# Optimization experiments

Measured on AMD Instinct MI355X. Metric: run time of the kernel, lower is better.

## Reference

```python
import jax, jax.numpy as jnp
import numpy as np
from jax import lax

B = 8192
HS = 64        # hidden_size (output channels)
HS4 = HS + 4   # internal channel count (68)
K = 3          # conv kernel size


def setup_inputs() -> dict:
    key = jax.random.key(0)
    ks = jax.random.split(key, 16)
    def n(k, shape, s=1.0):
        return jax.random.normal(k, shape, dtype=jnp.float32) * s
    return {
        "x": n(ks[0], (B, HS, 6, 6)),
        "cell": n(ks[1], (B, 2)),
        "interspace_coord": n(ks[2], (B, 2, 6, 6)),
        "conv1_w": n(ks[3], (HS4, HS4, K, K), 0.05),
        "conv1_b": n(ks[4], (HS4,), 0.05),
        "conv3_w": n(ks[5], (HS4, HS4, K, K), 0.05),
        "conv3_b": n(ks[6], (HS4,), 0.05),
        "lin5_w": n(ks[7], (9 * HS, HS4 * 25), 0.02),
        "lin5_b": n(ks[8], (9 * HS,), 0.02),
        "lin4_w": n(ks[9], (9 * HS, HS4 * 16), 0.02),
        "lin4_b": n(ks[10], (9 * HS,), 0.02),
        "lin3_w": n(ks[11], (9 * HS, HS4 * 9), 0.02),
        "lin3_b": n(ks[12], (9 * HS,), 0.02),
        "final_w": n(ks[13], (HS, 9 * HS), 0.02),
        "final_b": n(ks[14], (HS,), 0.02),
    }


def _conv(z, w, b):
    # torch Conv2d with padding=k//2, stride 1 == SAME conv, NCHW/OIHW
    y = lax.conv_general_dilated(z, w, (1, 1), 'SAME',
                                 dimension_numbers=('NCHW', 'OIHW', 'NCHW'))
    return y + b[None, :, None, None]


def _corners(z, ws):
    # four corner windows, stacked on a new leading axis (corner-major)
    H, W = z.shape[-2:]
    return jnp.stack([z[..., :ws, :ws],
                      z[..., :ws, W - ws:],
                      z[..., H - ws:, :ws],
                      z[..., H - ws:, W - ws:]], axis=0)


def reference(x, cell, interspace_coord,
              conv1_w, conv1_b, conv3_w, conv3_b,
              lin5_w, lin5_b, lin4_w, lin4_b, lin3_w, lin3_b,
              final_w, final_b):
    Bn = x.shape[0]
    new_cell = jnp.broadcast_to(cell.reshape(Bn, -1)[:, :, None, None],
                                (Bn, 2, 6, 6))
    lins = {5: (lin5_w, lin5_b), 4: (lin4_w, lin4_b), 3: (lin3_w, lin3_b)}
    for ws in (5, 4, 3):
        z = jnp.concatenate([x, new_cell, interspace_coord], axis=1)  # [B,68,6,6]
        z = _corners(z, ws).reshape(-1, HS4, ws, ws)                  # [4B,68,ws,ws]
        z = jnp.sin(z) + jnp.cos(z)
        z = jax.nn.relu(_conv(z, conv1_w, conv1_b))
        z = jnp.sin(z) + jnp.cos(z)
        z = jax.nn.relu(_conv(z, conv3_w, conv3_b)).reshape(4, Bn, -1)
        Wl, bl = lins[ws]
        z = jax.nn.relu(z @ Wl.T + bl).reshape(4, Bn, HS, 3, 3)
        m = jnp.concatenate([z[0], z[1]], axis=-1)   # [B,64,3,6]
        n = jnp.concatenate([z[2], z[3]], axis=-1)
        x = jnp.concatenate([m, n], axis=-2)          # [B,64,6,6]
    ew = 3
    c = _corners(x, ew)                               # [4,B,64,3,3]
    c = c.reshape(4 * Bn, -1) @ final_w.T + final_b   # [4B,64]
    c = c.reshape(Bn, HS, 2, 2)                       # same flat-order reshape as torch
    xc = x[:, :, ew - 1:ew + 1, ew - 1:ew + 1]        # center 2x2
    return (xc * c).reshape(Bn, HS, -1)
```

## Files before the change

### kernel.cpp

```cpp
#include <hip/hip_runtime.h>
#include <hip/hip_bf16.h>
#include <cstdint>
#include <cstddef>

#define BN 8192
#define MTOT 32768

using bf16 = __hip_bfloat16;
typedef float f32x4 __attribute__((ext_vector_type(4)));
typedef short short8 __attribute__((ext_vector_type(8)));

__device__ __forceinline__ bf16 f2b(float v) { return __float2bfloat16(v); }
__device__ __forceinline__ float b2f(bf16 v) { return __bfloat162float(v); }
__device__ __forceinline__ float sincos_sum(float x) {
    return 1.41421356237f * __sinf(x + 0.78539816340f);
}


__global__ __launch_bounds__(256)
void zprep_block(const float* __restrict__ xF, const float* __restrict__ cell,
                 const float* __restrict__ isc, bf16* __restrict__ Z,
                 int m0g, int CM)
{
    constexpr int KD = 1728, KTRUE = 1700;
    const int b = blockIdx.x, tid = threadIdx.x;
    __shared__ float s[68][37];

    for (int i = tid; i < 64 * 36; i += 256) {
        int ic = i / 36, off = i % 36;
        s[ic][off] = sincos_sum(xF[((size_t)b * 64 + ic) * 36 + off]);
    }
    if (tid < 2) {
        float t = sincos_sum(cell[b * 2 + tid]);
        #pragma unroll
        for (int off = 0; off < 36; off++) s[64 + tid][off] = t;
    }
    if (tid >= 64 && tid < 136) {
        int j = tid - 64;
        int ic = j / 36, off = j % 36;
        s[66 + ic][off] = sincos_sum(isc[((size_t)b * 2 + ic) * 36 + off]);
    }
    __syncthreads();

    for (int i = tid; i < 4 * (KD / 8); i += 256) {
        int q = i / (KD / 8), j8 = i % (KD / 8);
        int gm = q * BN + b;
        if (gm < m0g || gm >= m0g + CM) continue;
        int kbase = j8 * 8;
        short8 pack;
        #pragma unroll
        for (int u = 0; u < 8; u++) {
            int k = kbase + u;
            float v = 0.f;
            if (k < KTRUE) {
                int pi = k / 68, ic = k % 68;
                int r = (q >> 1) + pi / 5;
                int c = (q & 1) + pi % 5;
                v = s[ic][r * 6 + c];
            }
            bf16 bv = f2b(v);
            pack[u] = *reinterpret_cast<short*>(&bv);
        }
        *reinterpret_cast<short8*>(&Z[(size_t)(gm - m0g) * KD + kbase]) = pack;
    }
}

template<int WSv>
__device__ __forceinline__ bf16 conv_elem(const float* __restrict__ src, int n, int k)
{
    constexpr int KTRUE = 68 * WSv * WSv;
    float v = 0.f;
    if (n < KTRUE && k < KTRUE) {
        int po = n / 68, oc = n % 68, ro = po / WSv, co = po % WSv;
        int pi = k / 68, ic = k % 68, ri = pi / WSv, ci = pi % WSv;
        int kr = ri - ro + 1, kc = ci - co + 1;
        if (kr >= 0 && kr < 3 && kc >= 0 && kc < 3)
            v = src[((oc * 68 + ic) * 3 + kr) * 3 + kc];
    }
    return f2b(v);
}
template<int WSv>
__device__ __forceinline__ bf16 lin_elem(const float* __restrict__ wl, int n, int k)
{
    constexpr int KTRUE = 68 * WSv * WSv;
    float v = 0.f;
    if (n < 576 && k < KTRUE) {
        int pi = k / 68, ic = k % 68;
        v = wl[(size_t)n * KTRUE + ic * (WSv * WSv) + pi];
    }
    return f2b(v);
}

__global__ void megabuild(const float* __restrict__ c1w, const float* __restrict__ c3w,
                          const float* __restrict__ l5w, const float* __restrict__ l4w,
                          const float* __restrict__ l3w, const float* __restrict__ fw,
                          const float* __restrict__ c1b, const float* __restrict__ c3b,
                          const float* __restrict__ bl5, const float* __restrict__ bl4,
                          const float* __restrict__ bl3, const float* __restrict__ bfin,
                          const float* __restrict__ cell, const float* __restrict__ isc,
                          bf16* __restrict__ w1d5, bf16* __restrict__ w3d5,
                          bf16* __restrict__ w1d4, bf16* __restrict__ w3d4,
                          bf16* __restrict__ w1d3, bf16* __restrict__ w3d3,
                          bf16* __restrict__ wl5p, bf16* __restrict__ wl4p,
                          bf16* __restrict__ wl3p, bf16* __restrict__ wfp,
                          float* __restrict__ bias,
                          bf16* __restrict__ Z4, bf16* __restrict__ Z3)
{
    constexpr unsigned S0 = 2u*1792*1728, S1 = 2u*1152*1088, S2 = 2u*640*640;
    constexpr unsigned S3 = 640u*1728, S4 = 640u*1088, S5 = 640u*640;
    constexpr unsigned S6 = 128u*576, S7 = 9216;
    constexpr unsigned S8 = 4u*8192*16*4, S9 = 4u*8192*9*4, S10 = 32768u*28;
    constexpr unsigned O1=S0, O2=O1+S1, O3=O2+S2, O4=O3+S3, O5=O4+S4, O6=O5+S5,
                       O7=O6+S6, O8=O7+S7, O9=O8+S8, O10=O9+S9, OT=O10+S10;
    unsigned e = blockIdx.x * 256u + threadIdx.x;
    if (e >= OT) return;
    if (e < O1) {
        constexpr unsigned per = 1792u*1728;
        unsigned i = (e < per) ? e : e - per;
        bf16* dst = (e < per) ? w1d5 : w3d5;
        const float* src = (e < per) ? c1w : c3w;
        dst[i] = conv_elem<5>(src, (int)(i / 1728u), (int)(i % 1728u));
    } else if (e < O2) {
        unsigned i0 = e - O1; constexpr unsigned per = 1152u*1088;
        unsigned i = (i0 < per) ? i0 : i0 - per;
        bf16* dst = (i0 < per) ? w1d4 : w3d4;
        const float* src = (i0 < per) ? c1w : c3w;
        dst[i] = conv_elem<4>(src, (int)(i / 1088u), (int)(i % 1088u));
    } else if (e < O3) {
        unsigned i0 = e - O2; constexpr unsigned per = 640u*640;
        unsigned i = (i0 < per) ? i0 : i0 - per;
        bf16* dst = (i0 < per) ? w1d3 : w3d3;
        const float* src = (i0 < per) ? c1w : c3w;
        dst[i] = conv_elem<3>(src, (int)(i / 640u), (int)(i % 640u));
    } else if (e < O4) {
        unsigned i = e - O3;
        wl5p[i] = lin_elem<5>(l5w, (int)(i / 1728u), (int)(i % 1728u));
    } else if (e < O5) {
        unsigned i = e - O4;
        wl4p[i] = lin_elem<4>(l4w, (int)(i / 1088u), (int)(i % 1088u));
    } else if (e < O6) {
        unsigned i = e - O5;
        wl3p[i] = lin_elem<3>(l3w, (int)(i / 640u), (int)(i % 640u));
    } else if (e < O7) {
        unsigned i = e - O6, n = i / 576u, k = i % 576u;
        wfp[i] = (n < 64u) ? f2b(fw[n * 576u + k]) : f2b(0.f);
    } else if (e < O8) {
        int i = (int)(e - O7);
        float v = 0.f;
        if (i < 1792)      { int n = i;        if (n < 1700) v = c1b[n % 68]; }
        else if (i < 3584) { int n = i - 1792; if (n < 1700) v = c3b[n % 68]; }
        else if (i < 4736) { int n = i - 3584; if (n < 1088) v = c1b[n % 68]; }
        else if (i < 5888) { int n = i - 4736; if (n < 1088) v = c3b[n % 68]; }
        else if (i < 6528) { int n = i - 5888; if (n < 612)  v = c1b[n % 68]; }
        else if (i < 7168) { int n = i - 6528; if (n < 612)  v = c3b[n % 68]; }
        else if (i < 7808) { int n = i - 7168; if (n < 576)  v = bl5[n]; }
        else if (i < 8448) { int n = i - 7808; if (n < 576)  v = bl4[n]; }
        else if (i < 9088) { int n = i - 8448; if (n < 576)  v = bl3[n]; }
        else               { int n = i - 9088; if (n < 64)   v = bfin[n]; }
        bias[i] = v;
    } else if (e < O9) {
        unsigned i = e - O8;
        int j = (int)(i & 3u); i >>= 2;
        int pi = (int)(i & 15u); i >>= 4;
        int b = (int)(i & 8191u); int q = (int)(i >> 13);
        float t;
        if (j < 2) t = cell[b * 2 + j];
        else {
            int r = (q >> 1) * 2 + pi / 4, c = (q & 1) * 2 + pi % 4;
            t = isc[((size_t)b * 2 + (j - 2)) * 36 + r * 6 + c];
        }
        Z4[((size_t)q * BN + b) * 1088 + pi * 68 + 64 + j] = f2b(sincos_sum(t));
    } else if (e < O10) {
        unsigned i = e - O9;
        int j = (int)(i & 3u); i >>= 2;
        int pi = (int)(i % 9u); i /= 9u;
        int b = (int)(i & 8191u); int q = (int)(i >> 13);
        float t;
        if (j < 2) t = cell[b * 2 + j];
        else {
            int r = (q >> 1) * 3 + pi / 3, c = (q & 1) * 3 + pi % 3;
            t = isc[((size_t)b * 2 + (j - 2)) * 36 + r * 6 + c];
        }
        Z3[((size_t)q * BN + b) * 640 + pi * 68 + 64 + j] = f2b(sincos_sum(t));
    } else {
        unsigned i = e - O10;
        int m = (int)(i / 28u), t = (int)(i % 28u);
        Z3[(size_t)m * 640 + 612 + t] = f2b(0.f);
    }
}

__device__ __forceinline__ void gload_lds16(const bf16* g, const bf16* lds_wave_base)
{
    unsigned off = (unsigned)(uintptr_t)lds_wave_base;
    off = __builtin_amdgcn_readfirstlane(off);
    __builtin_amdgcn_global_load_lds((const __attribute__((address_space(1))) unsigned int*)g,
                                     (__attribute__((address_space(3))) unsigned int*)off,
                                     16, 0, 0);
}

__device__ __forceinline__ int imin(int a, int b) { return a < b ? a : b; }
__device__ __forceinline__ int imax(int a, int b) { return a > b ? a : b; }

template<int EPI, int WS, int WN, int WIDE>
__global__ __launch_bounds__(512, 4)
void gemm8(const bf16* __restrict__ A, const bf16* __restrict__ Bm, int KD,
           const float* __restrict__ bias, int ntiles, int mtiles,
           bf16* __restrict__ C, int ldc, int nlimit,
           int m0g, bf16* __restrict__ znext)
{
    constexpr int BMc = WIDE ? 128 : 256;
    constexpr int BNc = WIDE ? 256 : 128;
    constexpr int NWN = WIDE ? 4 : 2;
    __shared__ bf16 As[3][BMc * 32];
    __shared__ bf16 Bs[3][BNc * 32];
    const int tid = threadIdx.x;
    const int wave = tid >> 6, lane = tid & 63;
    const int l15 = lane & 15, lq = lane >> 4;
    const int wr = (wave / NWN) * 64, wc = (wave % NWN) * 64;

    const int xcd = blockIdx.x & 7, local = blockIdx.x >> 3;
    const int mloc = mtiles >> 3;
    const int PP = (mloc >= 4) ? 4 : mloc;
    const int grp = ntiles * PP;
    const int p = local / grp, rem = local % grp;
    const int n_idx = rem / PP, mi = rem % PP;
    const int m_idx = xcd * mloc + p * PP + mi;
    const int n0 = n_idx * BNc, m0 = m_idx * BMc;

    int s0b = 0, s0e = KD, s1b = 0, s1e = 0, s2b = 0, s2e = 0;
    if (WS > 0) {
        int po_lo = imin(n0 / 68, WS * WS - 1);
        int po_hi = imin((n0 + BNc - 1) / 68, WS * WS - 1);
        int ro_lo = po_lo / WS, ro_hi = po_hi / WS;
        int r_lo = imax(ro_lo - 1, 0), r_hi = imin(ro_hi + 1, WS - 1);
        int ci_lo = 0, ci_hi = WS - 1;
        if (ro_lo == ro_hi) {
            ci_lo = imax(po_lo % WS - 1, 0);
            ci_hi = imin(po_hi % WS + 1, WS - 1);
        }
        if (ci_lo == 0 && ci_hi == WS - 1) {
            s0b = (r_lo * WS * 68) & ~31;
            s0e = imin(KD, ((r_hi + 1) * WS * 68 + 31) & ~31);
        } else {
            s0b = ((r_lo * WS + ci_lo) * 68) & ~31;
            s0e = imin(KD, (((r_lo * WS + ci_hi + 1) * 68) + 31) & ~31);
            if (r_hi > r_lo) {
                s1b = (((r_lo + 1) * WS + ci_lo) * 68) & ~31;
                s1e = imin(KD, ((((r_lo + 1) * WS + ci_hi + 1) * 68) + 31) & ~31);
            }
            if (r_hi > r_lo + 1) {
                s2b = (((r_lo + 2) * WS + ci_lo) * 68) & ~31;
                s2e = imin(KD, ((((r_lo + 2) * WS + ci_hi + 1) * 68) + 31) & ~31);
            }
        }
    }
    const int c0 = (s0e - s0b) >> 5;
    const int c1 = c0 + ((s1e - s1b) >> 5);
    const int nt = c1 + ((s2e - s2b) >> 5);
    auto k0_of = [&](int t2) -> int {
        int k = s0b + (t2 << 5);
        if (t2 >= c0) k = s1b + ((t2 - c0) << 5);
        if (t2 >= c1) k = s2b + ((t2 - c1) << 5);
        return k;
    };

    const int srow = tid >> 2;
    const int scx = (tid & 3) ^ ((srow >> 1) & 3);
    const int sOff = srow * 32 + (tid & 3) * 8;
    const int swz = (lq ^ ((l15 >> 1) & 3)) * 8;
    const int offA0 = (wr + l15) * 32 + swz;
    const int offB0 = (wc + l15) * 32 + swz;

    const bf16* aSrc = A + (size_t)(m0 + srow) * KD + scx * 8;
    const bf16* bSrc = Bm + (size_t)(n0 + srow) * KD + scx * 8;

    auto stageAll = [&](int k0, int buf) {
        if (WIDE) {
            gload_lds16(aSrc + k0, &As[buf][sOff]);
            gload_lds16(bSrc + k0, &Bs[buf][sOff]);
            gload_lds16(bSrc + k0 + (size_t)128 * KD, &Bs[buf][sOff + 4096]);
        } else {
            gload_lds16(aSrc + k0, &As[buf][sOff]);
            gload_lds16(aSrc + k0 + (size_t)128 * KD, &As[buf][sOff + 4096]);
            gload_lds16(bSrc + k0, &Bs[buf][sOff]);
        }
    };

    f32x4 acc[4][4];
    #pragma unroll
    for (int i = 0; i < 4; i++)
        #pragma unroll
        for (int j = 0; j < 4; j++) { f32x4 z = {0.f, 0.f, 0.f, 0.f}; acc[i][j] = z; }

    {
        stageAll(k0_of(0), 0);
        if (nt > 1) stageAll(k0_of(1), 1);
        __syncthreads();
    }

    for (int t = 0; t < nt; ++t) {
        const int cur = t % 3;
        const int nx = (t + 2) % 3;
        const bool pf = (t + 2) < nt;

        const bf16* Ac = &As[cur][0];
        const bf16* Bc = &Bs[cur][0];

        short8 af[4], bg[4];
        #pragma unroll
        for (int i = 0; i < 4; i++) af[i] = *(const short8*)&Ac[offA0 + i * 512];
        #pragma unroll
        for (int j = 0; j < 4; j++) bg[j] = *(const short8*)&Bc[offB0 + j * 512];

        if (pf) stageAll(k0_of(t + 2), nx);

        __builtin_amdgcn_s_setprio(1);
        #pragma unroll
        for (int i = 0; i < 4; i++)
            #pragma unroll
            for (int j = 0; j < 4; j++)
                acc[i][j] = __builtin_amdgcn_mfma_f32_16x16x32_bf16(af[i], bg[j], acc[i][j], 0, 0, 0);
        __builtin_amdgcn_s_setprio(0);

        if (pf) asm volatile("s_waitcnt vmcnt(3)" ::: "memory");
        else    asm volatile("s_waitcnt vmcnt(0)" ::: "memory");
        __builtin_amdgcn_s_barrier();
    }

    float bj[4];
    #pragma unroll
    for (int j = 0; j < 4; j++) bj[j] = bias[n0 + wc + j * 16 + l15];

    #pragma unroll
    for (int i = 0; i < 4; i++) {
        #pragma unroll
        for (int j = 0; j < 4; j++) {
            int n = n0 + wc + j * 16 + l15;
            #pragma unroll
            for (int r = 0; r < 4; r++) {
                int m = m0 + wr + i * 16 + lq * 4 + r;
                float v = acc[i][j][r];
                if (EPI == 0) {
                    if (n < nlimit) {
                        v += bj[j]; v = fmaxf(v, 0.f); v = sincos_sum(v);
                        C[(size_t)m * ldc + n] = f2b(v);
                    }
                } else if (EPI == 1) {
                    if (n < nlimit) {
                        v += bj[j]; v = fmaxf(v, 0.f);
                        C[(size_t)m * ldc + n] = f2b(v);
                    }
                } else {
                    if (n < 576) {
                        v += bj[j]; v = fmaxf(v, 0.f);
                        bf16 tv = f2b(sincos_sum(v));
                        int gm = m0g + m;
                        int q = gm >> 13, b = gm & (BN - 1);
                        int ch = n / 9, p2 = n % 9;
                        int R = p2 / 3 + (q >> 1) * 3, Cc = p2 % 3 + (q & 1) * 3;
                        constexpr int OFF = 6 - WN;
                        constexpr int KDN = (WN == 4) ? 1088 : 640;
                        #pragma unroll
                        for (int qr = 0; qr < 2; qr++) {
                            int rr = R - OFF * qr;
                            if (rr < 0 || rr >= WN) continue;
                            #pragma unroll
                            for (int qc = 0; qc < 2; qc++) {
                                int cc = Cc - OFF * qc;
                                if (cc < 0 || cc >= WN) continue;
                                int pi = rr * WN + cc;
                                znext[((size_t)((qr * 2 + qc) * BN + b)) * KDN + pi * 68 + ch] = tv;
                            }
                        }
                    }
                }
            }
        }
    }
}

template<int EPI, int WS, int WN>
__global__ __launch_bounds__(256)
void gemm_bt(const bf16* __restrict__ A, const bf16* __restrict__ Bm, int KD,
             const float* __restrict__ bias, int ntiles,
             bf16* __restrict__ C, int ldc, int nlimit,
             int m0g, bf16* __restrict__ znext,
             const bf16* __restrict__ afin_xc, float* __restrict__ outp)
{
    __shared__ bf16 As[128 * 32];
    __shared__ bf16 Bs[128 * 32];
    const int tid = threadIdx.x;
    const int wave = tid >> 6, lane = tid & 63;
    const int l15 = lane & 15, lq = lane >> 4;
    const int wr = (wave >> 1) * 64, wc = (wave & 1) * 64;

    const int id = blockIdx.x;
    const int mt8 = (int)gridDim.x / (ntiles * 8);
    const int xcd = id & 7, local = id >> 3;
    const int m_idx = xcd * mt8 + local / ntiles;
    const int n_idx = local % ntiles;
    const int n0 = n_idx * 128, m0 = m_idx * 128;

    int nspans = 1, sbeg[4], send[4];
    sbeg[0] = 0; send[0] = KD;
    if (WS > 0) {
        int po_lo = imin(n0 / 68, WS * WS - 1);
        int po_hi = imin((n0 + 127) / 68, WS * WS - 1);
        int ro_lo = po_lo / WS, ro_hi = po_hi / WS;
        int r_lo = imax(ro_lo - 1, 0), r_hi = imin(ro_hi + 1, WS - 1);
        int ci_lo = 0, ci_hi = WS - 1;
        if (ro_lo == ro_hi) {
            ci_lo = imax(po_lo % WS - 1, 0);
            ci_hi = imin(po_hi % WS + 1, WS - 1);
        }
        if (ci_lo == 0 && ci_hi == WS - 1) {
            sbeg[0] = (r_lo * WS * 68) & ~31;
            send[0] = imin(KD, ((r_hi + 1) * WS * 68 + 31) & ~31);
        } else {
            nspans = 0;
            for (int ri = r_lo; ri <= r_hi; ri++) {
                sbeg[nspans] = ((ri * WS + ci_lo) * 68) & ~31;
                send[nspans] = imin(KD, (((ri * WS + ci_hi + 1) * 68) + 31) & ~31);
                nspans++;
            }
        }
    }

    float bj[4];
    #pragma unroll
    for (int j = 0; j < 4; j++) bj[j] = bias[n0 + wc + j * 16 + l15];

    const bf16* Ab = A + (size_t)m0 * KD;
    const bf16* Bb = Bm + (size_t)n0 * KD;
    const int srow = tid >> 2, scol = (tid & 3) * 8;
    const bf16* aG0 = Ab + (size_t)srow * KD + scol;
    const bf16* aG1 = Ab + (size_t)(srow + 64) * KD + scol;
    const bf16* bG0 = Bb + (size_t)srow * KD + scol;
    const bf16* bG1 = Bb + (size_t)(srow + 64) * KD + scol;
    const bf16* lA0 = &As[wave * 512];
    const bf16* lA1 = &As[2048 + wave * 512];
    const bf16* lB0 = &Bs[wave * 512];
    const bf16* lB1 = &Bs[2048 + wave * 512];

    f32x4 acc[4][4];
    #pragma unroll
    for (int i = 0; i < 4; i++)
        #pragma unroll
        for (int j = 0; j < 4; j++) { f32x4 z = {0.f, 0.f, 0.f, 0.f}; acc[i][j] = z; }

    for (int s = 0; s < nspans; s++) {
        for (int k0 = sbeg[s]; k0 < send[s]; k0 += 32) {
            gload_lds16(aG0 + k0, lA0);
            gload_lds16(aG1 + k0, lA1);
            gload_lds16(bG0 + k0, lB0);
            gload_lds16(bG1 + k0, lB1);
            __syncthreads();
            short8 af[4], bg[4];
            #pragma unroll
            for (int i = 0; i < 4; i++) af[i] = *(const short8*)&As[(wr + i * 16 + l15) * 32 + lq * 8];
            #pragma unroll
            for (int j = 0; j < 4; j++) bg[j] = *(const short8*)&Bs[(wc + j * 16 + l15) * 32 + lq * 8];
            #pragma unroll
            for (int i = 0; i < 4; i++)
                #pragma unroll
                for (int j = 0; j < 4; j++)
                    acc[i][j] = __builtin_amdgcn_mfma_f32_16x16x32_bf16(af[i], bg[j], acc[i][j], 0, 0, 0);
            __syncthreads();
        }
    }

    #pragma unroll
    for (int i = 0; i < 4; i++) {
        #pragma unroll
        for (int j = 0; j < 4; j++) {
            int n = n0 + wc + j * 16 + l15;
            #pragma unroll
            for (int r = 0; r < 4; r++) {
                int m = m0 + wr + i * 16 + lq * 4 + r;
                float v = acc[i][j][r];
                if (EPI == 0) {
                    if (n < nlimit) {
                        v += bj[j]; v = fmaxf(v, 0.f); v = sincos_sum(v);
                        C[(size_t)m * ldc + n] = f2b(v);
                    }
                } else if (EPI == 1) {
                    if (n < nlimit) {
                        v += bj[j]; v = fmaxf(v, 0.f);
                        C[(size_t)m * ldc + n] = f2b(v);
                    }
                } else if (EPI == 2) {
                    if (n < 576) {
                        v += bj[j]; v = fmaxf(v, 0.f);
                        bf16 t = f2b(sincos_sum(v));
                        int gm = m0g + m;
                        int q = gm >> 13, b = gm & (BN - 1);
                        int ch = n / 9, p = n % 9;
                        int R = p / 3 + (q >> 1) * 3, Cc = p % 3 + (q & 1) * 3;
                        constexpr int OFF = 6 - WN;
                        constexpr int KDN = (WN == 4) ? 1088 : 640;
                        #pragma unroll
                        for (int qr = 0; qr < 2; qr++) {
                            int rr = R - OFF * qr;
                            if (rr < 0 || rr >= WN) continue;
                            #pragma unroll
                            for (int qc = 0; qc < 2; qc++) {
                                int cc = Cc - OFF * qc;
                                if (cc < 0 || cc >= WN) continue;
                                int pi = rr * WN + cc;
                                znext[((size_t)((qr * 2 + qc) * BN + b)) * KDN + pi * 68 + ch] = t;
                            }
                        }
                    }
                } else {
                    if (n < 64) {
                        v += bj[j];
                        int gm = m0g + m;
                        int f = gm * 64 + n;
                        int b2 = f >> 8, rem = f & 255;
                        int ch2 = rem >> 2, ii = (rem >> 1) & 1, jj = rem & 1;
                        int qq = ii * 2 + jj;
                        const int offt[4] = {8, 6, 2, 0};
                        float xc = b2f(afin_xc[((size_t)qq * BN + b2) * 576 + ch2 * 9 + offt[qq]]);
                        outp[f] = v * xc;
                    }
                }
            }
        }
    }
}

extern "C" void kernel_launch(void* const* d_in, const int* in_sizes, int n_in,
                              void* d_out, int out_size, void* d_ws, size_t ws_size,
                              hipStream_t stream)
{
    const float* x    = (const float*)d_in[0];
    const float* cell = (const float*)d_in[1];
    const float* isc  = (const float*)d_in[2];
    const float* c1w  = (const float*)d_in[3];
    const float* c1b  = (const float*)d_in[4];
    const float* c3w  = (const float*)d_in[5];
    const float* c3b  = (const float*)d_in[6];
    const float* l5w  = (const float*)d_in[7];
    const float* l5b  = (const float*)d_in[8];
    const float* l4w  = (const float*)d_in[9];
    const float* l4b  = (const float*)d_in[10];
    const float* l3w  = (const float*)d_in[11];
    const float* l3b  = (const float*)d_in[12];
    const float* fw   = (const float*)d_in[13];
    const float* fb   = (const float*)d_in[14];

    char* base = (char*)d_ws;
    size_t cur = 0;
    auto take = [&](size_t bytes) -> char* {
        char* r = base + cur; cur += (bytes + 255) & ~(size_t)255; return r;
    };

    const size_t Z4B = (size_t)MTOT * 1088 * 2;
    const size_t Z3B = (size_t)MTOT * 640 * 2;
    const size_t AFB = (size_t)MTOT * 576 * 2;
    size_t wbytes = 2 * (1792ull * 1728 + 1152ull * 1088 + 640ull * 640) * 2
                  + (640ull * 1728 + 640ull * 1088 + 640ull * 640) * 2
                  + 128ull * 576 * 2 + 9216ull * 4 + 64 * 256;
    auto need = [&](int nc) -> size_t {
        return Z4B + Z3B + AFB + wbytes + 2 * ((size_t)(MTOT / nc) * 1728 * 2);
    };
    int nchunk = (ws_size >= need(1)) ? 1 : (ws_size >= need(2)) ? 2
               : (ws_size >= need(4)) ? 4 : (ws_size >= need(8)) ? 8 : 16;

    bf16* Z4   = (bf16*)take(Z4B);
    bf16* Z3   = (bf16*)take(Z3B);
    bf16* afinb = (bf16*)take(AFB);
    bf16* w1d5 = (bf16*)take(1792ull * 1728 * 2);
    bf16* w3d5 = (bf16*)take(1792ull * 1728 * 2);
    bf16* w1d4 = (bf16*)take(1152ull * 1088 * 2);
    bf16* w3d4 = (bf16*)take(1152ull * 1088 * 2);
    bf16* w1d3 = (bf16*)take(640ull * 640 * 2);
    bf16* w3d3 = (bf16*)take(640ull * 640 * 2);
    bf16* wl5p = (bf16*)take(640ull * 1728 * 2);
    bf16* wl4p = (bf16*)take(640ull * 1088 * 2);
    bf16* wl3p = (bf16*)take(640ull * 640 * 2);
    bf16* wfp  = (bf16*)take(128ull * 576 * 2);
    float* biasb = (float*)take(9216ull * 4);
    int CM = MTOT / nchunk;
    int mt = CM / 128;
    int mt2 = CM / 256;
    bf16* Za = (bf16*)take((size_t)CM * 1728 * 2);
    bf16* Zb = (bf16*)take((size_t)CM * 1728 * 2);

    {
        constexpr unsigned OT = 2u*1792*1728 + 2u*1152*1088 + 2u*640*640
                              + 640u*1728 + 640u*1088 + 640u*640 + 128u*576 + 9216
                              + 4u*8192*16*4 + 4u*8192*9*4 + 32768u*28;
        megabuild<<<(OT + 255) / 256, 256, 0, stream>>>(
            c1w, c3w, l5w, l4w, l3w, fw, c1b, c3b, l5b, l4b, l3b, fb, cell, isc,
            w1d5, w3d5, w1d4, w3d4, w1d3, w3d3, wl5p, wl4p, wl3p, wfp, biasb, Z4, Z3);
    }

    for (int c = 0; c < nchunk; c++) {
        int m0g = c * CM;
        zprep_block<<<BN, 256, 0, stream>>>(x, cell, isc, Za, m0g, CM);
        gemm8<0, 5, 0, 1><<<7 * mt, 512, 0, stream>>>(Za, w1d5, 1728, biasb + 0, 7, mt,
                                                      Zb, 1728, 1728, 0, nullptr);
        gemm8<1, 5, 0, 1><<<7 * mt, 512, 0, stream>>>(Zb, w3d5, 1728, biasb + 1792, 7, mt,
                                                      Za, 1728, 1728, 0, nullptr);
        gemm8<2, 0, 4, 0><<<5 * mt2, 512, 0, stream>>>(Za, wl5p, 1728, biasb + 7168, 5, mt2,
                                                       nullptr, 0, 0, m0g, Z4);
    }
    for (int c = 0; c < nchunk; c++) {
        int m0g = c * CM;
        gemm8<0, 4, 0, 0><<<9 * mt2, 512, 0, stream>>>(Z4 + (size_t)m0g * 1088, w1d4, 1088,
                                                       biasb + 3584, 9, mt2, Zb, 1088, 1088,
                                                       0, nullptr);
        gemm8<1, 4, 0, 0><<<9 * mt2, 512, 0, stream>>>(Zb, w3d4, 1088, biasb + 4736, 9, mt2,
                                                       Za, 1088, 1088, 0, nullptr);
        gemm8<2, 0, 3, 0><<<5 * mt2, 512, 0, stream>>>(Za, wl4p, 1088, biasb + 7808, 5, mt2,
                                                       nullptr, 0, 0, m0g, Z3);
    }
    for (int c = 0; c < nchunk; c++) {
        int m0g = c * CM;
        gemm8<0, 3, 0, 0><<<5 * mt2, 512, 0, stream>>>(Z3 + (size_t)m0g * 640, w1d3, 640,
                                                       biasb + 5888, 5, mt2, Zb, 640, 640,
                                                       0, nullptr);
        gemm8<1, 3, 0, 0><<<5 * mt2, 512, 0, stream>>>(Zb, w3d3, 640, biasb + 6528, 5, mt2,
                                                       Za, 640, 640, 0, nullptr);
        gemm8<1, 0, 0, 0><<<5 * mt2, 512, 0, stream>>>(Za, wl3p, 640, biasb + 8448, 5, mt2,
                                                       afinb + (size_t)m0g * 576, 576, 576,
                                                       0, nullptr);
    }
    for (int c = 0; c < nchunk; c++) {
        int m0g = c * CM;
        gemm_bt<3, 0, 0><<<mt, 256, 0, stream>>>(afinb + (size_t)m0g * 576, wfp, 576,
                                                 biasb + 9088, 1, nullptr, 0, 0, m0g,
                                                 nullptr, afinb, (float*)d_out);
    }
}
```

Before: 1.179 ms.

## Sub-chunk layer GEMM chain into row slices for cache locality when unchunked

When the whole batch is handled in one chunk, zprep still runs once over all rows. Each stage's conv1, conv3 and linear GEMM chain then runs over 8192-row slices, so the intermediate activations of a slice can stay resident in the large last-level cache between consecutive GEMMs. The aim is to cut HBM traffic between dependent launches. In exchange it launches more, smaller kernels, and each launch fills the GPU less.

Result: no change. 1.172 ms (-0.5%).

```diff
diff --git a/kernel.cpp b/kernel.cpp
--- a/kernel.cpp
+++ b/kernel.cpp
@@ -596,41 +596,91 @@
             w1d5, w3d5, w1d4, w3d4, w1d3, w3d3, wl5p, wl4p, wl3p, wfp, biasb, Z4, Z3);
     }
 
-    for (int c = 0; c < nchunk; c++) {
-        int m0g = c * CM;
-        zprep_block<<<BN, 256, 0, stream>>>(x, cell, isc, Za, m0g, CM);
-        gemm8<0, 5, 0, 1><<<7 * mt, 512, 0, stream>>>(Za, w1d5, 1728, biasb + 0, 7, mt,
-                                                      Zb, 1728, 1728, 0, nullptr);
-        gemm8<1, 5, 0, 1><<<7 * mt, 512, 0, stream>>>(Zb, w3d5, 1728, biasb + 1792, 7, mt,
-                                                      Za, 1728, 1728, 0, nullptr);
-        gemm8<2, 0, 4, 0><<<5 * mt2, 512, 0, stream>>>(Za, wl5p, 1728, biasb + 7168, 5, mt2,
-                                                       nullptr, 0, 0, m0g, Z4);
-    }
-    for (int c = 0; c < nchunk; c++) {
-        int m0g = c * CM;
-        gemm8<0, 4, 0, 0><<<9 * mt2, 512, 0, stream>>>(Z4 + (size_t)m0g * 1088, w1d4, 1088,
-                                                       biasb + 3584, 9, mt2, Zb, 1088, 1088,
-                                                       0, nullptr);
-        gemm8<1, 4, 0, 0><<<9 * mt2, 512, 0, stream>>>(Zb, w3d4, 1088, biasb + 4736, 9, mt2,
-                                                       Za, 1088, 1088, 0, nullptr);
-        gemm8<2, 0, 3, 0><<<5 * mt2, 512, 0, stream>>>(Za, wl4p, 1088, biasb + 7808, 5, mt2,
-                                                       nullptr, 0, 0, m0g, Z3);
-    }
-    for (int c = 0; c < nchunk; c++) {
-        int m0g = c * CM;
-        gemm8<0, 3, 0, 0><<<5 * mt2, 512, 0, stream>>>(Z3 + (size_t)m0g * 640, w1d3, 640,
-                                                       biasb + 5888, 5, mt2, Zb, 640, 640,
-                                                       0, nullptr);
-        gemm8<1, 3, 0, 0><<<5 * mt2, 512, 0, stream>>>(Zb, w3d3, 640, biasb + 6528, 5, mt2,
-                                                       Za, 640, 640, 0, nullptr);
-        gemm8<1, 0, 0, 0><<<5 * mt2, 512, 0, stream>>>(Za, wl3p, 640, biasb + 8448, 5, mt2,
-                                                       afinb + (size_t)m0g * 576, 576, 576,
-                                                       0, nullptr);
-    }
-    for (int c = 0; c < nchunk; c++) {
-        int m0g = c * CM;
-        gemm_bt<3, 0, 0><<<mt, 256, 0, stream>>>(afinb + (size_t)m0g * 576, wfp, 576,
-                                                 biasb + 9088, 1, nullptr, 0, 0, m0g,
-                                                 nullptr, afinb, (float*)d_out);
-    }
-}
+    if (nchunk == 1) {
+        constexpr int SM = 8192;
+        constexpr int NC = MTOT / SM;
+        const int smt = SM / 128;
+        const int smt2 = SM / 256;
+
+        zprep_block<<<BN, 256, 0, stream>>>(x, cell, isc, Za, 0, MTOT);
+
+        for (int cc = 0; cc < NC; cc++) {
+            size_t o5 = (size_t)cc * SM * 1728;
+            gemm8<0, 5, 0, 1><<<7 * smt, 512, 0, stream>>>(Za + o5, w1d5, 1728, biasb + 0,
+                                                           7, smt, Zb + o5, 1728, 1728,
+                                                           0, nullptr);
+            gemm8<1, 5, 0, 1><<<7 * smt, 512, 0, stream>>>(Zb + o5, w3d5, 1728, biasb + 1792,
+                                                           7, smt, Za + o5, 1728, 1728,
+                                                           0, nullptr);
+            gemm8<2, 0, 4, 0><<<5 * smt2, 512, 0, stream>>>(Za + o5, wl5p, 1728, biasb + 7168,
+                                                            5, smt2, nullptr, 0, 0,
+                                                            cc * SM, Z4);
+        }
+        for (int cc = 0; cc < NC; cc++) {
+            size_t o4 = (size_t)cc * SM * 1088;
+            gemm8<0, 4, 0, 0><<<9 * smt2, 512, 0, stream>>>(Z4 + o4, w1d4, 1088, biasb + 3584,
+                                                            9, smt2, (bf16*)((char*)Zb) + o4,
+                                                            1088, 1088, 0, nullptr);
+            gemm8<1, 4, 0, 0><<<9 * smt2, 512, 0, stream>>>(Zb + o4, w3d4, 1088, biasb + 4736,
+                                                            9, smt2, Za + o4, 1088, 1088,
+                                                            0, nullptr);
+            gemm8<2, 0, 3, 0><<<5 * smt2, 512, 0, stream>>>(Za + o4, wl4p, 1088, biasb + 7808,
+                                                            5, smt2, nullptr, 0, 0,
+                                                            cc * SM, Z3);
+        }
+        for (int cc = 0; cc < NC; cc++) {
+            size_t o3 = (size_t)cc * SM * 640;
+            gemm8<0, 3, 0, 0><<<5 * smt2, 512, 0, stream>>>(Z3 + o3, w1d3, 640, biasb + 5888,
+                                                            5, smt2, Zb + o3, 640, 640,
+                                                            0, nullptr);
+            gemm8<1, 3, 0, 0><<<5 * smt2, 512, 0, stream>>>(Zb + o3, w3d3, 640, biasb + 6528,
+                                                            5, smt2, Za + o3, 640, 640,
+                                                            0, nullptr);
+            gemm8<1, 0, 0, 0><<<5 * smt2, 512, 0, stream>>>(Za + o3, wl3p, 640, biasb + 8448,
+                                                            5, smt2,
+                                                            afinb + (size_t)cc * SM * 576,
+                                                            576, 576, 0, nullptr);
+        }
+        gemm_bt<3, 0, 0><<<mt, 256, 0, stream>>>(afinb, wfp, 576, biasb + 9088, 1,
+                                                 nullptr, 0, 0, 0, nullptr, afinb,
+                                                 (float*)d_out);
+    } else {
+        for (int c = 0; c < nchunk; c++) {
+            int m0g = c * CM;
+            zprep_block<<<BN, 256, 0, stream>>>(x, cell, isc, Za, m0g, CM);
+            gemm8<0, 5, 0, 1><<<7 * mt, 512, 0, stream>>>(Za, w1d5, 1728, biasb + 0, 7, mt,
+                                                          Zb, 1728, 1728, 0, nullptr);
+            gemm8<1, 5, 0, 1><<<7 * mt, 512, 0, stream>>>(Zb, w3d5, 1728, biasb + 1792, 7, mt,
+                                                          Za, 1728, 1728, 0, nullptr);
+            gemm8<2, 0, 4, 0><<<5 * mt2, 512, 0, stream>>>(Za, wl5p, 1728, biasb + 7168, 5, mt2,
+                                                           nullptr, 0, 0, m0g, Z4);
+        }
+        for (int c = 0; c < nchunk; c++) {
+            int m0g = c * CM;
+            gemm8<0, 4, 0, 0><<<9 * mt2, 512, 0, stream>>>(Z4 + (size_t)m0g * 1088, w1d4, 1088,
+                                                           biasb + 3584, 9, mt2, Zb, 1088, 1088,
+                                                           0, nullptr);
+            gemm8<1, 4, 0, 0><<<9 * mt2, 512, 0, stream>>>(Zb, w3d4, 1088, biasb + 4736, 9, mt2,
+                                                           Za, 1088, 1088, 0, nullptr);
+            gemm8<2, 0, 3, 0><<<5 * mt2, 512, 0, stream>>>(Za, wl4p, 1088, biasb + 7808, 5, mt2,
+                                                           nullptr, 0, 0, m0g, Z3);
+        }
+        for (int c = 0; c < nchunk; c++) {
+            int m0g = c * CM;
+            gemm8<0, 3, 0, 0><<<5 * mt2, 512, 0, stream>>>(Z3 + (size_t)m0g * 640, w1d3, 640,
+                                                           biasb + 5888, 5, mt2, Zb, 640, 640,
+                                                           0, nullptr);
+            gemm8<1, 3, 0, 0><<<5 * mt2, 512, 0, stream>>>(Zb, w3d3, 640, biasb + 6528, 5, mt2,
+                                                           Za, 640, 640, 0, nullptr);
+            gemm8<1, 0, 0, 0><<<5 * mt2, 512, 0, stream>>>(Za, wl3p, 640, biasb + 8448, 5, mt2,
+                                                           afinb + (size_t)m0g * 576, 576, 576,
+                                                           0, nullptr);
+        }
+        for (int c = 0; c < nchunk; c++) {
+            int m0g = c * CM;
+            gemm_bt<3, 0, 0><<<mt, 256, 0, stream>>>(afinb + (size_t)m0g * 576, wfp, 576,
+                                                     biasb + 9088, 1, nullptr, 0, 0, m0g,
+                                                     nullptr, afinb, (float*)d_out);
+        }
+    }
+}
```

## Switch GEMMs to 256x256 tiles with a persistent grid-stride block loop

Applied to the files above, without the earlier changes.

Replaces the 128x256/256x128 tile GEMM with a 256x256 tile variant, where each wave computes a 64x128 sub-tile. Blocks now loop over tiles in a fixed 256-block persistent grid rather than one block per tile. Weight buffers are padded to multiples of 256 rows. The aim is more operand reuse per LDS load and less launch and tail overhead. In exchange it uses more registers and LDS per block, lowers the occupancy hint to 2, and wastes more MMA work on padded N rows for the smaller layers.

Result: slower. 1.353 ms (+14.8%).

```diff
diff --git a/kernel.cpp b/kernel.cpp
--- a/kernel.cpp
+++ b/kernel.cpp
@@ -201,68 +201,27 @@
 __device__ __forceinline__ int imin(int a, int b) { return a < b ? a : b; }
 __device__ __forceinline__ int imax(int a, int b) { return a > b ? a : b; }
 
-template<int EPI, int WS, int WN, int WIDE>
-__global__ __launch_bounds__(512, 4)
-void gemm8(const bf16* __restrict__ A, const bf16* __restrict__ Bm, int KD,
+template<int EPI, int WS, int WN>
+__global__ __launch_bounds__(512, 2)
+void gemm9(const bf16* __restrict__ A, const bf16* __restrict__ Bm, int KD,
            const float* __restrict__ bias, int ntiles, int mtiles,
            bf16* __restrict__ C, int ldc, int nlimit,
            int m0g, bf16* __restrict__ znext)
 {
-    constexpr int BMc = WIDE ? 128 : 256;
-    constexpr int BNc = WIDE ? 256 : 128;
-    constexpr int NWN = WIDE ? 4 : 2;
-    __shared__ bf16 As[3][BMc * 32];
-    __shared__ bf16 Bs[3][BNc * 32];
+    __shared__ bf16 As[3][8192];
+    __shared__ bf16 Bs[3][8192];
     const int tid = threadIdx.x;
     const int wave = tid >> 6, lane = tid & 63;
     const int l15 = lane & 15, lq = lane >> 4;
-    const int wr = (wave / NWN) * 64, wc = (wave % NWN) * 64;
-
-    const int xcd = blockIdx.x & 7, local = blockIdx.x >> 3;
+    const int wr = (wave >> 1) * 64;
+    const int wc = (wave & 1) * 128;
+
+    const int xcd = blockIdx.x & 7, lblk = blockIdx.x >> 3;
+    const int bpx = (int)gridDim.x >> 3;
     const int mloc = mtiles >> 3;
     const int PP = (mloc >= 4) ? 4 : mloc;
     const int grp = ntiles * PP;
-    const int p = local / grp, rem = local % grp;
-    const int n_idx = rem / PP, mi = rem % PP;
-    const int m_idx = xcd * mloc + p * PP + mi;
-    const int n0 = n_idx * BNc, m0 = m_idx * BMc;
-
-    int s0b = 0, s0e = KD, s1b = 0, s1e = 0, s2b = 0, s2e = 0;
-    if (WS > 0) {
-        int po_lo = imin(n0 / 68, WS * WS - 1);
-        int po_hi = imin((n0 + BNc - 1) / 68, WS * WS - 1);
-        int ro_lo = po_lo / WS, ro_hi = po_hi / WS;
-        int r_lo = imax(ro_lo - 1, 0), r_hi = imin(ro_hi + 1, WS - 1);
-        int ci_lo = 0, ci_hi = WS - 1;
-        if (ro_lo == ro_hi) {
-            ci_lo = imax(po_lo % WS - 1, 0);
-            ci_hi = imin(po_hi % WS + 1, WS - 1);
-        }
-        if (ci_lo == 0 && ci_hi == WS - 1) {
-            s0b = (r_lo * WS * 68) & ~31;
-            s0e = imin(KD, ((r_hi + 1) * WS * 68 + 31) & ~31);
-        } else {
-            s0b = ((r_lo * WS + ci_lo) * 68) & ~31;
-            s0e = imin(KD, (((r_lo * WS + ci_hi + 1) * 68) + 31) & ~31);
-            if (r_hi > r_lo) {
-                s1b = (((r_lo + 1) * WS + ci_lo) * 68) & ~31;
-                s1e = imin(KD, ((((r_lo + 1) * WS + ci_hi + 1) * 68) + 31) & ~31);
-            }
-            if (r_hi > r_lo + 1) {
-                s2b = (((r_lo + 2) * WS + ci_lo) * 68) & ~31;
-                s2e = imin(KD, ((((r_lo + 2) * WS + ci_hi + 1) * 68) + 31) & ~31);
-            }
-        }
-    }
-    const int c0 = (s0e - s0b) >> 5;
-    const int c1 = c0 + ((s1e - s1b) >> 5);
-    const int nt = c1 + ((s2e - s2b) >> 5);
-    auto k0_of = [&](int t2) -> int {
-        int k = s0b + (t2 << 5);
-        if (t2 >= c0) k = s1b + ((t2 - c0) << 5);
-        if (t2 >= c1) k = s2b + ((t2 - c1) << 5);
-        return k;
-    };
+    const int tot = mloc * ntiles;
 
     const int srow = tid >> 2;
     const int scx = (tid & 3) ^ ((srow >> 1) & 3);
@@ -271,105 +230,144 @@
     const int offA0 = (wr + l15) * 32 + swz;
     const int offB0 = (wc + l15) * 32 + swz;
 
-    const bf16* aSrc = A + (size_t)(m0 + srow) * KD + scx * 8;
-    const bf16* bSrc = Bm + (size_t)(n0 + srow) * KD + scx * 8;
-
-    auto stageAll = [&](int k0, int buf) {
-        if (WIDE) {
-            gload_lds16(aSrc + k0, &As[buf][sOff]);
-            gload_lds16(bSrc + k0, &Bs[buf][sOff]);
-            gload_lds16(bSrc + k0 + (size_t)128 * KD, &Bs[buf][sOff + 4096]);
-        } else {
+    for (int w = lblk; w < tot; w += bpx) {
+        const int p = w / grp, rem = w % grp;
+        const int n_idx = rem / PP, mi = rem % PP;
+        const int m_idx = xcd * mloc + p * PP + mi;
+        const int n0 = n_idx * 256, m0 = m_idx * 256;
+
+        int s0b = 0, s0e = KD, s1b = 0, s1e = 0, s2b = 0, s2e = 0;
+        if (WS > 0) {
+            int po_lo = imin(n0 / 68, WS * WS - 1);
+            int po_hi = imin((n0 + 255) / 68, WS * WS - 1);
+            int ro_lo = po_lo / WS, ro_hi = po_hi / WS;
+            int r_lo = imax(ro_lo - 1, 0), r_hi = imin(ro_hi + 1, WS - 1);
+            int ci_lo = 0, ci_hi = WS - 1;
+            if (ro_lo == ro_hi) {
+                ci_lo = imax(po_lo % WS - 1, 0);
+                ci_hi = imin(po_hi % WS + 1, WS - 1);
+            }
+            if (ci_lo == 0 && ci_hi == WS - 1) {
+                s0b = (r_lo * WS * 68) & ~31;
+                s0e = imin(KD, ((r_hi + 1) * WS * 68 + 31) & ~31);
+            } else {
+                s0b = ((r_lo * WS + ci_lo) * 68) & ~31;
+                s0e = imin(KD, (((r_lo * WS + ci_hi + 1) * 68) + 31) & ~31);
+                if (r_hi > r_lo) {
+                    s1b = (((r_lo + 1) * WS + ci_lo) * 68) & ~31;
+                    s1e = imin(KD, ((((r_lo + 1) * WS + ci_hi + 1) * 68) + 31) & ~31);
+                }
+                if (r_hi > r_lo + 1) {
+                    s2b = (((r_lo + 2) * WS + ci_lo) * 68) & ~31;
+                    s2e = imin(KD, ((((r_lo + 2) * WS + ci_hi + 1) * 68) + 31) & ~31);
+                }
+            }
+        }
+        const int c0 = (s0e - s0b) >> 5;
+        const int c1 = c0 + ((s1e - s1b) >> 5);
+        const int nt = c1 + ((s2e - s2b) >> 5);
+        auto k0_of = [&](int t2) -> int {
+            int k = s0b + (t2 << 5);
+            if (t2 >= c0) k = s1b + ((t2 - c0) << 5);
+            if (t2 >= c1) k = s2b + ((t2 - c1) << 5);
+            return k;
+        };
+
+        const bf16* aSrc = A + (size_t)(m0 + srow) * KD + scx * 8;
+        const bf16* bSrc = Bm + (size_t)(n0 + srow) * KD + scx * 8;
+
+        auto stageAll = [&](int k0, int buf) {
             gload_lds16(aSrc + k0, &As[buf][sOff]);
             gload_lds16(aSrc + k0 + (size_t)128 * KD, &As[buf][sOff + 4096]);
             gload_lds16(bSrc + k0, &Bs[buf][sOff]);
-        }
-    };
-
-    f32x4 acc[4][4];
-    #pragma unroll
-    for (int i = 0; i < 4; i++)
-        #pragma unroll
-        for (int j = 0; j < 4; j++) { f32x4 z = {0.f, 0.f, 0.f, 0.f}; acc[i][j] = z; }
-
-    {
-        stageAll(k0_of(0), 0);
-        if (nt > 1) stageAll(k0_of(1), 1);
-        __syncthreads();
-    }
-
-    for (int t = 0; t < nt; ++t) {
-        const int cur = t % 3;
-        const int nx = (t + 2) % 3;
-        const bool pf = (t + 2) < nt;
-
-        const bf16* Ac = &As[cur][0];
-        const bf16* Bc = &Bs[cur][0];
-
-        short8 af[4], bg[4];
-        #pragma unroll
-        for (int i = 0; i < 4; i++) af[i] = *(const short8*)&Ac[offA0 + i * 512];
-        #pragma unroll
-        for (int j = 0; j < 4; j++) bg[j] = *(const short8*)&Bc[offB0 + j * 512];
-
-        if (pf) stageAll(k0_of(t + 2), nx);
-
-        __builtin_amdgcn_s_setprio(1);
+            gload_lds16(bSrc + k0 + (size_t)128 * KD, &Bs[buf][sOff + 4096]);
+        };
+
+        f32x4 acc[4][8];
         #pragma unroll
         for (int i = 0; i < 4; i++)
             #pragma unroll
-            for (int j = 0; j < 4; j++)
-                acc[i][j] = __builtin_amdgcn_mfma_f32_16x16x32_bf16(af[i], bg[j], acc[i][j], 0, 0, 0);
-        __builtin_amdgcn_s_setprio(0);
-
-        if (pf) asm volatile("s_waitcnt vmcnt(3)" ::: "memory");
-        else    asm volatile("s_waitcnt vmcnt(0)" ::: "memory");
-        __builtin_amdgcn_s_barrier();
-    }
-
-    float bj[4];
-    #pragma unroll
-    for (int j = 0; j < 4; j++) bj[j] = bias[n0 + wc + j * 16 + l15];
-
-    #pragma unroll
-    for (int i = 0; i < 4; i++) {
+            for (int j = 0; j < 8; j++) { f32x4 z = {0.f, 0.f, 0.f, 0.f}; acc[i][j] = z; }
+
+        {
+            stageAll(k0_of(0), 0);
+            if (nt > 1) stageAll(k0_of(1), 1);
+            __syncthreads();
+        }
+
+        for (int t = 0; t < nt; ++t) {
+            const int cur = t % 3;
+            const int nx = (t + 2) % 3;
+            const bool pf = (t + 2) < nt;
+
+            const bf16* Ac = &As[cur][0];
+            const bf16* Bc = &Bs[cur][0];
+
+            short8 af[4], bg[8];
+            #pragma unroll
+            for (int i = 0; i < 4; i++) af[i] = *(const short8*)&Ac[offA0 + i * 512];
+            #pragma unroll
+            for (int j = 0; j < 8; j++) bg[j] = *(const short8*)&Bc[offB0 + j * 512];
+
+            if (pf) stageAll(k0_of(t + 2), nx);
+
+            __builtin_amdgcn_s_setprio(1);
+            #pragma unroll
+            for (int i = 0; i < 4; i++)
+                #pragma unroll
+                for (int j = 0; j < 8; j++)
+                    acc[i][j] = __builtin_amdgcn_mfma_f32_16x16x32_bf16(af[i], bg[j], acc[i][j], 0, 0, 0);
+            __builtin_amdgcn_s_setprio(0);
+
+            if (pf) asm volatile("s_waitcnt vmcnt(4)" ::: "memory");
+            else    asm volatile("s_waitcnt vmcnt(0)" ::: "memory");
+            __builtin_amdgcn_s_barrier();
+        }
+
+        float bj[8];
         #pragma unroll
-        for (int j = 0; j < 4; j++) {
-            int n = n0 + wc + j * 16 + l15;
-            #pragma unroll
-            for (int r = 0; r < 4; r++) {
-                int m = m0 + wr + i * 16 + lq * 4 + r;
-                float v = acc[i][j][r];
-                if (EPI == 0) {
-                    if (n < nlimit) {
-                        v += bj[j]; v = fmaxf(v, 0.f); v = sincos_sum(v);
-                        C[(size_t)m * ldc + n] = f2b(v);
-                    }
-                } else if (EPI == 1) {
-                    if (n < nlimit) {
-                        v += bj[j]; v = fmaxf(v, 0.f);
-                        C[(size_t)m * ldc + n] = f2b(v);
-                    }
-                } else {
-                    if (n < 576) {
-                        v += bj[j]; v = fmaxf(v, 0.f);
-                        bf16 tv = f2b(sincos_sum(v));
-                        int gm = m0g + m;
-                        int q = gm >> 13, b = gm & (BN - 1);
-                        int ch = n / 9, p2 = n % 9;
-                        int R = p2 / 3 + (q >> 1) * 3, Cc = p2 % 3 + (q & 1) * 3;
-                        constexpr int OFF = 6 - WN;
-                        constexpr int KDN = (WN == 4) ? 1088 : 640;
-                        #pragma unroll
-                        for (int qr = 0; qr < 2; qr++) {
-                            int rr = R - OFF * qr;
-                            if (rr < 0 || rr >= WN) continue;
+        for (int j = 0; j < 8; j++) bj[j] = bias[n0 + wc + j * 16 + l15];
+
+        #pragma unroll
+        for (int i = 0; i < 4; i++) {
+            #pragma unroll
+            for (int j = 0; j < 8; j++) {
+                int n = n0 + wc + j * 16 + l15;
+                #pragma unroll
+                for (int r = 0; r < 4; r++) {
+                    int m = m0 + wr + i * 16 + lq * 4 + r;
+                    float v = acc[i][j][r];
+                    if (EPI == 0) {
+                        if (n < nlimit) {
+                            v += bj[j]; v = fmaxf(v, 0.f); v = sincos_sum(v);
+                            C[(size_t)m * ldc + n] = f2b(v);
+                        }
+                    } else if (EPI == 1) {
+                        if (n < nlimit) {
+                            v += bj[j]; v = fmaxf(v, 0.f);
+                            C[(size_t)m * ldc + n] = f2b(v);
+                        }
+                    } else {
+                        if (n < 576) {
+                            v += bj[j]; v = fmaxf(v, 0.f);
+                            bf16 tv = f2b(sincos_sum(v));
+                            int gm = m0g + m;
+                            int q = gm >> 13, b = gm & (BN - 1);
+                            int ch = n / 9, p2 = n % 9;
+                            int R = p2 / 3 + (q >> 1) * 3, Cc = p2 % 3 + (q & 1) * 3;
+                            constexpr int OFF = 6 - WN;
+                            constexpr int KDN = (WN == 4) ? 1088 : 640;
                             #pragma unroll
-                            for (int qc = 0; qc < 2; qc++) {
-                                int cc = Cc - OFF * qc;
-                                if (cc < 0 || cc >= WN) continue;
-                                int pi = rr * WN + cc;
-                                znext[((size_t)((qr * 2 + qc) * BN + b)) * KDN + pi * 68 + ch] = tv;
+                            for (int qr = 0; qr < 2; qr++) {
+                                int rr = R - OFF * qr;
+                                if (rr < 0 || rr >= WN) continue;
+                                #pragma unroll
+                                for (int qc = 0; qc < 2; qc++) {
+                                    int cc = Cc - OFF * qc;
+                                    if (cc < 0 || cc >= WN) continue;
+                                    int pi = rr * WN + cc;
+                                    znext[((size_t)((qr * 2 + qc) * BN + b)) * KDN + pi * 68 + ch] = tv;
+                                }
                             }
                         }
                     }
@@ -558,8 +556,8 @@
     const size_t Z4B = (size_t)MTOT * 1088 * 2;
     const size_t Z3B = (size_t)MTOT * 640 * 2;
     const size_t AFB = (size_t)MTOT * 576 * 2;
-    size_t wbytes = 2 * (1792ull * 1728 + 1152ull * 1088 + 640ull * 640) * 2
-                  + (640ull * 1728 + 640ull * 1088 + 640ull * 640) * 2
+    size_t wbytes = 2 * (1792ull * 1728 + 1280ull * 1088 + 768ull * 640) * 2
+                  + (768ull * 1728 + 768ull * 1088 + 768ull * 640) * 2
                   + 128ull * 576 * 2 + 9216ull * 4 + 64 * 256;
     auto need = [&](int nc) -> size_t {
         return Z4B + Z3B + AFB + wbytes + 2 * ((size_t)(MTOT / nc) * 1728 * 2);
@@ -572,18 +570,18 @@
     bf16* afinb = (bf16*)take(AFB);
     bf16* w1d5 = (bf16*)take(1792ull * 1728 * 2);
     bf16* w3d5 = (bf16*)take(1792ull * 1728 * 2);
-    bf16* w1d4 = (bf16*)take(1152ull * 1088 * 2);
-    bf16* w3d4 = (bf16*)take(1152ull * 1088 * 2);
-    bf16* w1d3 = (bf16*)take(640ull * 640 * 2);
-    bf16* w3d3 = (bf16*)take(640ull * 640 * 2);
-    bf16* wl5p = (bf16*)take(640ull * 1728 * 2);
-    bf16* wl4p = (bf16*)take(640ull * 1088 * 2);
-    bf16* wl3p = (bf16*)take(640ull * 640 * 2);
+    bf16* w1d4 = (bf16*)take(1280ull * 1088 * 2);
+    bf16* w3d4 = (bf16*)take(1280ull * 1088 * 2);
+    bf16* w1d3 = (bf16*)take(768ull * 640 * 2);
+    bf16* w3d3 = (bf16*)take(768ull * 640 * 2);
+    bf16* wl5p = (bf16*)take(768ull * 1728 * 2);
+    bf16* wl4p = (bf16*)take(768ull * 1088 * 2);
+    bf16* wl3p = (bf16*)take(768ull * 640 * 2);
     bf16* wfp  = (bf16*)take(128ull * 576 * 2);
     float* biasb = (float*)take(9216ull * 4);
     int CM = MTOT / nchunk;
     int mt = CM / 128;
-    int mt2 = CM / 256;
+    int mt256 = CM / 256;
     bf16* Za = (bf16*)take((size_t)CM * 1728 * 2);
     bf16* Zb = (bf16*)take((size_t)CM * 1728 * 2);
 
@@ -599,33 +597,33 @@
     for (int c = 0; c < nchunk; c++) {
         int m0g = c * CM;
         zprep_block<<<BN, 256, 0, stream>>>(x, cell, isc, Za, m0g, CM);
-        gemm8<0, 5, 0, 1><<<7 * mt, 512, 0, stream>>>(Za, w1d5, 1728, biasb + 0, 7, mt,
-                                                      Zb, 1728, 1728, 0, nullptr);
-        gemm8<1, 5, 0, 1><<<7 * mt, 512, 0, stream>>>(Zb, w3d5, 1728, biasb + 1792, 7, mt,
-                                                      Za, 1728, 1728, 0, nullptr);
-        gemm8<2, 0, 4, 0><<<5 * mt2, 512, 0, stream>>>(Za, wl5p, 1728, biasb + 7168, 5, mt2,
-                                                       nullptr, 0, 0, m0g, Z4);
+        gemm9<0, 5, 0><<<256, 512, 0, stream>>>(Za, w1d5, 1728, biasb + 0, 7, mt256,
+                                                Zb, 1728, 1728, 0, nullptr);
+        gemm9<1, 5, 0><<<256, 512, 0, stream>>>(Zb, w3d5, 1728, biasb + 1792, 7, mt256,
+                                                Za, 1728, 1728, 0, nullptr);
+        gemm9<2, 0, 4><<<256, 512, 0, stream>>>(Za, wl5p, 1728, biasb + 7168, 3, mt256,
+                                                nullptr, 0, 0, m0g, Z4);
     }
     for (int c = 0; c < nchunk; c++) {
         int m0g = c * CM;
-        gemm8<0, 4, 0, 0><<<9 * mt2, 512, 0, stream>>>(Z4 + (size_t)m0g * 1088, w1d4, 1088,
-                                                       biasb + 3584, 9, mt2, Zb, 1088, 1088,
-                                                       0, nullptr);
-        gemm8<1, 4, 0, 0><<<9 * mt2, 512, 0, stream>>>(Zb, w3d4, 1088, biasb + 4736, 9, mt2,
-                                                       Za, 1088, 1088, 0, nullptr);
-        gemm8<2, 0, 3, 0><<<5 * mt2, 512, 0, stream>>>(Za, wl4p, 1088, biasb + 7808, 5, mt2,
-                                                       nullptr, 0, 0, m0g, Z3);
+        gemm9<0, 4, 0><<<256, 512, 0, stream>>>(Z4 + (size_t)m0g * 1088, w1d4, 1088,
+                                                biasb + 3584, 5, mt256, Zb, 1088, 1088,
+                                                0, nullptr);
+        gemm9<1, 4, 0><<<256, 512, 0, stream>>>(Zb, w3d4, 1088, biasb + 4736, 5, mt256,
+                                                Za, 1088, 1088, 0, nullptr);
+        gemm9<2, 0, 3><<<256, 512, 0, stream>>>(Za, wl4p, 1088, biasb + 7808, 3, mt256,
+                                                nullptr, 0, 0, m0g, Z3);
     }
     for (int c = 0; c < nchunk; c++) {
         int m0g = c * CM;
-        gemm8<0, 3, 0, 0><<<5 * mt2, 512, 0, stream>>>(Z3 + (size_t)m0g * 640, w1d3, 640,
-                                                       biasb + 5888, 5, mt2, Zb, 640, 640,
-                                                       0, nullptr);
-        gemm8<1, 3, 0, 0><<<5 * mt2, 512, 0, stream>>>(Zb, w3d3, 640, biasb + 6528, 5, mt2,
-                                                       Za, 640, 640, 0, nullptr);
-        gemm8<1, 0, 0, 0><<<5 * mt2, 512, 0, stream>>>(Za, wl3p, 640, biasb + 8448, 5, mt2,
-                                                       afinb + (size_t)m0g * 576, 576, 576,
-                                                       0, nullptr);
+        gemm9<0, 3, 0><<<256, 512, 0, stream>>>(Z3 + (size_t)m0g * 640, w1d3, 640,
+                                                biasb + 5888, 3, mt256, Zb, 640, 640,
+                                                0, nullptr);
+        gemm9<1, 3, 0><<<256, 512, 0, stream>>>(Zb, w3d3, 640, biasb + 6528, 3, mt256,
+                                                Za, 640, 640, 0, nullptr);
+        gemm9<1, 0, 0><<<256, 512, 0, stream>>>(Za, wl3p, 640, biasb + 8448, 3, mt256,
+                                                afinb + (size_t)m0g * 576, 576, 576,
+                                                0, nullptr);
     }
     for (int c = 0; c < nchunk; c++) {
         int m0g = c * CM;
```
